# Optimization experiments

Measured on AMD Instinct MI355X. Metric: run time of the kernel, lower is better.

Reference implementation:

```python
import jax, jax.numpy as jnp
import numpy as np


def setup_inputs() -> dict:
    key = jax.random.key(0)
    k1, k2 = jax.random.split(key)
    B, N, M, D = 8, 8192, 8192, 3
    input1 = jax.random.normal(k1, (B, N, D), dtype=jnp.float32)
    input2 = jax.random.normal(k2, (B, M, D), dtype=jnp.float32)
    return {"input1": input1, "input2": input2}


def reference(input1, input2):
    # input1: [B, N, 3], input2: [B, M, 3]
    # Squared pairwise distances via ||x||^2 + ||y||^2 - 2<x,y>
    sq1 = jnp.sum(input1 * input1, axis=-1)          # [B, N]
    sq2 = jnp.sum(input2 * input2, axis=-1)          # [B, M]
    inner = jnp.einsum('bnd,bmd->bnm', input1, input2)  # [B, N, M]
    d = sq1[:, :, None] + sq2[:, None, :] - 2.0 * inner  # [B, N, M]
    d = jnp.maximum(d, 0.0)  # numerical guard
    dist1 = jnp.min(d, axis=2)  # [B, N] NN in input2 for each point of input1
    dist2 = jnp.min(d, axis=1)  # [B, M] NN in input1 for each point of input2
    loss = jnp.mean(dist1) + jnp.mean(dist2)
    return loss
```

## Files before the change

kernel.cpp:

```cpp
#include <hip/hip_runtime.h>


typedef _Float16 half8 __attribute__((ext_vector_type(8)));
typedef float    f16x  __attribute__((ext_vector_type(16)));

constexpr int B       = 8;
constexpr int NPTS    = 8192;
constexpr int TOTAL   = B * NPTS;
constexpr int NSTRIP  = 256;
constexpr int NSTRIPS = NPTS / NSTRIP;
constexpr int MH      = 4;
constexpr int MHALF   = NPTS / MH;
constexpr int CHUNK   = 512;
constexpr int NCHUNK  = MHALF / CHUNK;

__device__ __forceinline__ void packB(float cx, float cy, float cz,
                                      half8& plo, half8& phi)
{
    float x = -2.f * cx, y = -2.f * cy, z = -2.f * cz;
    float sq = fmaf(cx, cx, fmaf(cy, cy, cz * cz));
    _Float16 xh = (_Float16)x, yh = (_Float16)y, zh = (_Float16)z;
    _Float16 xl = (_Float16)(x - (float)xh);
    _Float16 yl = (_Float16)(y - (float)yh);
    _Float16 zl = (_Float16)(z - (float)zh);
    _Float16 sh = (_Float16)sq, sl = (_Float16)(sq - (float)sh);
    plo = half8{xh, yh, zh, xh, yh, zh, xl, yl};
    phi = half8{zl, (_Float16)1.f, (_Float16)1.f, sh, sl,
                (_Float16)0.f, (_Float16)0.f, (_Float16)0.f};
}

__global__ __launch_bounds__(512, 8) void nn_mfma(
    const float* __restrict__ in1, const float* __restrict__ in2,
    float* __restrict__ minp, float* __restrict__ out)
{
    const int b     = blockIdx.z;
    const int strip = blockIdx.x;
    const int pass  = blockIdx.y / MH;
    const int mh    = blockIdx.y % MH;
    const int wave  = threadIdx.x >> 6;
    const int lane  = threadIdx.x & 63;
    const int col   = lane & 31;
    const int half  = lane >> 5;

    const float* Apts = pass ? in2 : in1;
    const float* Bpts = pass ? in1 : in2;

    if ((blockIdx.x | blockIdx.y | blockIdx.z) == 0 && threadIdx.x == 0)
        *out = 0.0f;

    __shared__ _Float16 ldsB[CHUNK * 16];

    const int nbase = strip * NSTRIP + wave * 32;
    half8 afrag;
    {
        const float* a = Apts + ((size_t)b * NPTS + nbase + col) * 3;
        float x = a[0], y = a[1], z = a[2];
        float sq = fmaf(x, x, fmaf(y, y, z * z));
        _Float16 xh = (_Float16)x, yh = (_Float16)y, zh = (_Float16)z;
        _Float16 xl = (_Float16)(x - (float)xh);
        _Float16 yl = (_Float16)(y - (float)yh);
        _Float16 zl = (_Float16)(z - (float)zh);
        _Float16 sh = (_Float16)sq, sl = (_Float16)(sq - (float)sh);
        half8 lo = {xh, yh, zh, xl, yl, zl, xh, yh};
        half8 hi = {zh, sh, sl, (_Float16)1.f, (_Float16)1.f,
                    (_Float16)0.f, (_Float16)0.f, (_Float16)0.f};
        afrag = half ? hi : lo;
    }

    f16x MN1, zacc;
#pragma unroll
    for (int r = 0; r < 16; ++r) { MN1[r] = 1e30f; zacc[r] = 0.0f; }

    const float* Craw = Bpts + ((size_t)b * NPTS + mh * MHALF) * 3;

    float px, py, pz;
    {
        const float* cp = Craw + (size_t)threadIdx.x * 3;
        px = cp[0]; py = cp[1]; pz = cp[2];
    }

    for (int c = 0; c < NCHUNK; ++c) {
        half8 plo, phi;
        packB(px, py, pz, plo, phi);
        __syncthreads();
        *(half8*)&ldsB[(threadIdx.x >> 5) * 512 + (threadIdx.x & 31) * 8]       = plo;
        *(half8*)&ldsB[(threadIdx.x >> 5) * 512 + 256 + (threadIdx.x & 31) * 8] = phi;
        if (c + 1 < NCHUNK) {
            const float* cp = Craw + (size_t)((c + 1) * CHUNK + threadIdx.x) * 3;
            px = cp[0]; py = cp[1]; pz = cp[2];
        }
        __syncthreads();

#pragma unroll
        for (int t = 0; t < CHUNK / 32; t += 2) {
            half8 bfA = *(const half8*)&ldsB[ t      * 512 + lane * 8];
            half8 bfB = *(const half8*)&ldsB[(t + 1) * 512 + lane * 8];
            f16x accA = __builtin_amdgcn_mfma_f32_32x32x16_f16(afrag, bfA, zacc, 0, 0, 0);
            f16x accB = __builtin_amdgcn_mfma_f32_32x32x16_f16(afrag, bfB, zacc, 0, 0, 0);

#pragma unroll
            for (int r = 0; r < 16; ++r)
                MN1[r] = fminf(fminf(accA[r], accB[r]), MN1[r]);
        }
    }

#pragma unroll
    for (int m = 1; m <= 16; m <<= 1)
#pragma unroll
        for (int r = 0; r < 16; ++r)
            MN1[r] = fminf(MN1[r], __shfl_xor(MN1[r], m, 64));
    if (col == 0) {
        float* o = minp + (((size_t)pass * B + b) * MH + mh) * NPTS + nbase;
#pragma unroll
        for (int r = 0; r < 16; ++r)
            o[(r & 3) + 8 * (r >> 2) + 4 * half] = MN1[r];
    }
}

__global__ __launch_bounds__(64) void reduce_kernel(
    const float* __restrict__ minp, float* __restrict__ out)
{
    int g  = blockIdx.x * 64 + threadIdx.x;
    int b  = g >> 11;
    int mq = g & 2047;

    float v = 0.0f;
#pragma unroll
    for (int p = 0; p < 2; ++p) {
        const float4* pp =
            (const float4*)(minp + (((size_t)p * B + b) * MH) * NPTS) + mq;
        float4 a = pp[0];
#pragma unroll
        for (int s = 1; s < MH; ++s) {
            float4 t = pp[(size_t)s * (NPTS / 4)];
            a.x = fminf(a.x, t.x); a.y = fminf(a.y, t.y);
            a.z = fminf(a.z, t.z); a.w = fminf(a.w, t.w);
        }
        v += fmaxf(a.x, 0.0f) + fmaxf(a.y, 0.0f)
           + fmaxf(a.z, 0.0f) + fmaxf(a.w, 0.0f);
    }

#pragma unroll
    for (int off = 32; off; off >>= 1)
        v += __shfl_down(v, off, 64);
    if (threadIdx.x == 0)
        atomicAdd(out, v * (1.0f / (float)TOTAL));
}

extern "C" void kernel_launch(void* const* d_in, const int* in_sizes, int n_in,
                              void* d_out, int out_size, void* d_ws, size_t ws_size,
                              hipStream_t stream)
{
    const float* in1 = (const float*)d_in[0];
    const float* in2 = (const float*)d_in[1];
    float* out = (float*)d_out;

    float* minp = (float*)d_ws;

    nn_mfma<<<dim3(NSTRIPS, 2 * MH, B), 512, 0, stream>>>(
        in1, in2, minp, out);
    reduce_kernel<<<TOTAL / 4 / 64, 64, 0, stream>>>(minp, out);
}
```

Before: 105.1 us.

## Register-block two A fragments per wave and double LDS chunk size

Each wave now holds two 32-point A fragments and computes a 2x2 block of MFMAs per pair of B fragments loaded from LDS, so each LDS read is reused twice. The strip per block grows to 512 points and the staged chunk to 1024 points, halving the number of sync rounds and the block count. This raises register and LDS use (launch bounds drop to 4 blocks per CU) and halves grid parallelism, which may reduce occupancy and latency hiding.

Measured after the change: 100.3 us. 4.5% less time.

```diff
diff --git a/kernel.cpp b/kernel.cpp
--- a/kernel.cpp
+++ b/kernel.cpp
@@ -7,11 +7,11 @@
 constexpr int B       = 8;
 constexpr int NPTS    = 8192;
 constexpr int TOTAL   = B * NPTS;
-constexpr int NSTRIP  = 256;
+constexpr int NSTRIP  = 512;
 constexpr int NSTRIPS = NPTS / NSTRIP;
 constexpr int MH      = 4;
 constexpr int MHALF   = NPTS / MH;
-constexpr int CHUNK   = 512;
+constexpr int CHUNK   = 1024;
 constexpr int NCHUNK  = MHALF / CHUNK;
 
 __device__ __forceinline__ void packB(float cx, float cy, float cz,
@@ -29,7 +29,7 @@
                 (_Float16)0.f, (_Float16)0.f, (_Float16)0.f};
 }
 
-__global__ __launch_bounds__(512, 8) void nn_mfma(
+__global__ __launch_bounds__(512, 4) void nn_mfma(
     const float* __restrict__ in1, const float* __restrict__ in2,
     float* __restrict__ minp, float* __restrict__ out)
 {
@@ -50,10 +50,11 @@
 
     __shared__ _Float16 ldsB[CHUNK * 16];
 
-    const int nbase = strip * NSTRIP + wave * 32;
-    half8 afrag;
-    {
-        const float* a = Apts + ((size_t)b * NPTS + nbase + col) * 3;
+    const int nbase = strip * NSTRIP + wave * 64;
+    half8 afrag0, afrag1;
+#pragma unroll
+    for (int s = 0; s < 2; ++s) {
+        const float* a = Apts + ((size_t)b * NPTS + nbase + s * 32 + col) * 3;
         float x = a[0], y = a[1], z = a[2];
         float sq = fmaf(x, x, fmaf(y, y, z * z));
         _Float16 xh = (_Float16)x, yh = (_Float16)y, zh = (_Float16)z;
@@ -64,56 +65,76 @@
         half8 lo = {xh, yh, zh, xl, yl, zl, xh, yh};
         half8 hi = {zh, sh, sl, (_Float16)1.f, (_Float16)1.f,
                     (_Float16)0.f, (_Float16)0.f, (_Float16)0.f};
-        afrag = half ? hi : lo;
+        if (s == 0) afrag0 = half ? hi : lo;
+        else        afrag1 = half ? hi : lo;
     }
 
-    f16x MN1, zacc;
+    f16x MN1a, MN1b, zacc;
 #pragma unroll
-    for (int r = 0; r < 16; ++r) { MN1[r] = 1e30f; zacc[r] = 0.0f; }
+    for (int r = 0; r < 16; ++r) { MN1a[r] = 1e30f; MN1b[r] = 1e30f; zacc[r] = 0.0f; }
 
     const float* Craw = Bpts + ((size_t)b * NPTS + mh * MHALF) * 3;
 
-    float px, py, pz;
+    float px0, py0, pz0, px1, py1, pz1;
     {
         const float* cp = Craw + (size_t)threadIdx.x * 3;
-        px = cp[0]; py = cp[1]; pz = cp[2];
+        px0 = cp[0]; py0 = cp[1]; pz0 = cp[2];
+        const float* cq = Craw + (size_t)(512 + threadIdx.x) * 3;
+        px1 = cq[0]; py1 = cq[1]; pz1 = cq[2];
     }
 
     for (int c = 0; c < NCHUNK; ++c) {
-        half8 plo, phi;
-        packB(px, py, pz, plo, phi);
+        half8 plo0, phi0, plo1, phi1;
+        packB(px0, py0, pz0, plo0, phi0);
+        packB(px1, py1, pz1, plo1, phi1);
         __syncthreads();
-        *(half8*)&ldsB[(threadIdx.x >> 5) * 512 + (threadIdx.x & 31) * 8]       = plo;
-        *(half8*)&ldsB[(threadIdx.x >> 5) * 512 + 256 + (threadIdx.x & 31) * 8] = phi;
+        {
+            const int i0 = threadIdx.x;
+            const int i1 = threadIdx.x + 512;
+            *(half8*)&ldsB[(i0 >> 5) * 512 + (i0 & 31) * 8]       = plo0;
+            *(half8*)&ldsB[(i0 >> 5) * 512 + 256 + (i0 & 31) * 8] = phi0;
+            *(half8*)&ldsB[(i1 >> 5) * 512 + (i1 & 31) * 8]       = plo1;
+            *(half8*)&ldsB[(i1 >> 5) * 512 + 256 + (i1 & 31) * 8] = phi1;
+        }
         if (c + 1 < NCHUNK) {
             const float* cp = Craw + (size_t)((c + 1) * CHUNK + threadIdx.x) * 3;
-            px = cp[0]; py = cp[1]; pz = cp[2];
+            px0 = cp[0]; py0 = cp[1]; pz0 = cp[2];
+            const float* cq = Craw + (size_t)((c + 1) * CHUNK + 512 + threadIdx.x) * 3;
+            px1 = cq[0]; py1 = cq[1]; pz1 = cq[2];
         }
         __syncthreads();
 
 #pragma unroll
         for (int t = 0; t < CHUNK / 32; t += 2) {
-            half8 bfA = *(const half8*)&ldsB[ t      * 512 + lane * 8];
-            half8 bfB = *(const half8*)&ldsB[(t + 1) * 512 + lane * 8];
-            f16x accA = __builtin_amdgcn_mfma_f32_32x32x16_f16(afrag, bfA, zacc, 0, 0, 0);
-            f16x accB = __builtin_amdgcn_mfma_f32_32x32x16_f16(afrag, bfB, zacc, 0, 0, 0);
+            half8 bf0 = *(const half8*)&ldsB[ t      * 512 + lane * 8];
+            half8 bf1 = *(const half8*)&ldsB[(t + 1) * 512 + lane * 8];
+            f16x acc00 = __builtin_amdgcn_mfma_f32_32x32x16_f16(afrag0, bf0, zacc, 0, 0, 0);
+            f16x acc01 = __builtin_amdgcn_mfma_f32_32x32x16_f16(afrag0, bf1, zacc, 0, 0, 0);
+            f16x acc10 = __builtin_amdgcn_mfma_f32_32x32x16_f16(afrag1, bf0, zacc, 0, 0, 0);
+            f16x acc11 = __builtin_amdgcn_mfma_f32_32x32x16_f16(afrag1, bf1, zacc, 0, 0, 0);
 
 #pragma unroll
-            for (int r = 0; r < 16; ++r)
-                MN1[r] = fminf(fminf(accA[r], accB[r]), MN1[r]);
+            for (int r = 0; r < 16; ++r) {
+                MN1a[r] = fminf(fminf(acc00[r], acc01[r]), MN1a[r]);
+                MN1b[r] = fminf(fminf(acc10[r], acc11[r]), MN1b[r]);
+            }
         }
     }
 
 #pragma unroll
     for (int m = 1; m <= 16; m <<= 1)
 #pragma unroll
-        for (int r = 0; r < 16; ++r)
-            MN1[r] = fminf(MN1[r], __shfl_xor(MN1[r], m, 64));
+        for (int r = 0; r < 16; ++r) {
+            MN1a[r] = fminf(MN1a[r], __shfl_xor(MN1a[r], m, 64));
+            MN1b[r] = fminf(MN1b[r], __shfl_xor(MN1b[r], m, 64));
+        }
     if (col == 0) {
         float* o = minp + (((size_t)pass * B + b) * MH + mh) * NPTS + nbase;
 #pragma unroll
-        for (int r = 0; r < 16; ++r)
-            o[(r & 3) + 8 * (r >> 2) + 4 * half] = MN1[r];
+        for (int r = 0; r < 16; ++r) {
+            o[(r & 3) + 8 * (r >> 2) + 4 * half]      = MN1a[r];
+            o[32 + (r & 3) + 8 * (r >> 2) + 4 * half] = MN1b[r];
+        }
     }
 }
 
```
